# Kernel optimization log

Hardware: AMD Instinct MI355X
Metric: run time of the kernel (lower is better)

## Reference

```python
import jax, jax.numpy as jnp
import numpy as np

P, Q, R, H1, H2, PH, B = 32, 32, 8, 128, 64, 16, 8192
PAIRS = P * Q
OUT = PAIRS * R  # X_Z_layer output units


def _pairwise_mask(p, q, r):
    # rows i*q+k correspond to pair (x_i, z_k): connected to x_i and z_k only
    mx = np.zeros((p * q, p), np.float32)
    for i in range(p):
        mx[i * q:(i + 1) * q, i] = 1.0
    mz = np.tile(np.eye(q, dtype=np.float32), (p, 1))
    m = np.concatenate([mx, mz], axis=1)          # [p*q, p+q]
    return np.repeat(m, r, axis=0)                 # [p*q*r, p+q]


def setup_inputs() -> dict:
    key = jax.random.key(0)
    ks = jax.random.split(key, 24)
    rn = lambda k, s, sc=0.1: jax.random.normal(k, s, jnp.float32) * sc
    x = jax.random.normal(ks[0], (B, P), jnp.float32)
    z = jax.random.normal(ks[1], (B, Q), jnp.float32)
    # X_mlp: P -> H1 -> H2 -> 1
    xw1, xb1 = rn(ks[2], (P, H1)), rn(ks[3], (H1,))
    xw2, xb2 = rn(ks[4], (H1, H2)), rn(ks[5], (H2,))
    xw3, xb3 = rn(ks[6], (H2, 1)), rn(ks[7], (1,))
    # Z_mlp: Q -> H1 -> H2 -> 1
    zw1, zb1 = rn(ks[8], (Q, H1)), rn(ks[9], (H1,))
    zw2, zb2 = rn(ks[10], (Q if False else H1, H2)), rn(ks[11], (H2,))
    zw3, zb3 = rn(ks[12], (H2, 1)), rn(ks[13], (1,))
    # masked X_Z_layer: weight pre-multiplied by structured mask (as in __init__)
    mask = jnp.asarray(_pairwise_mask(P, Q, R))    # [OUT, P+Q]
    xzw = (rn(ks[14], (OUT, P + Q)) * mask).T      # [P+Q, OUT]
    xzb = rn(ks[15], (OUT,))
    # 1024 tiny per-pair MLPs: R -> PH (bias) -> 1 (no bias), stacked
    pw1 = rn(ks[16], (PAIRS, R, PH))
    pb1 = rn(ks[17], (PAIRS, PH))
    pw2 = rn(ks[18], (PAIRS, PH))
    return dict(x=x, z=z, xw1=xw1, xb1=xb1, xw2=xw2, xb2=xb2, xw3=xw3, xb3=xb3,
                zw1=zw1, zb1=zb1, zw2=zw2, zb2=zb2, zw3=zw3, zb3=zb3,
                xzw=xzw, xzb=xzb, pw1=pw1, pb1=pb1, pw2=pw2)


def reference(x, z, xw1, xb1, xw2, xb2, xw3, xb3,
              zw1, zb1, zw2, zb2, zw3, zb3, xzw, xzb, pw1, pb1, pw2):
    relu = jax.nn.relu
    # main-effect MLPs
    hx = relu(relu(x @ xw1 + xb1) @ xw2 + xb2)
    out_x = hx @ xw3 + xb3                         # [B,1]
    hz = relu(relu(z @ zw1 + zb1) @ zw2 + zb2)
    out_z = hz @ zw3 + zb3                         # [B,1]
    # masked interaction layer
    xz = jnp.concatenate([x, z], axis=1)           # [B, P+Q]
    h = relu(xz @ xzw + xzb)                       # [B, OUT]
    # all 1024 per-pair MLPs as one batched GEMM
    hp = h.reshape(h.shape[0], PAIRS, R)           # [B, pairs, R]
    t = relu(jnp.einsum('bpr,prh->bph', hp, pw1) + pb1)
    out_xz = jnp.einsum('bph,ph->b', t, pw2)[:, None]  # sum over pairs -> [B,1]
    return out_x + out_z + out_xz
```

## Files before the change

### kernel.cpp

```cpp
#include <hip/hip_runtime.h>

#define B_TOT 8192
#define PP 32
#define QQ 32
#define RR 8
#define H1 128
#define H2 64
#define PHH 16
#define PAIRS 1024
#define OUT_UNITS 8192

#define NBLK_MM 256
#define NBLK_IA 2048

typedef float f32x16 __attribute__((ext_vector_type(16)));
typedef short s16x8  __attribute__((ext_vector_type(8)));

union FragU { s16x8 v; unsigned int u[4]; };

__device__ inline unsigned int pack_bf16(float lo, float hi) {
    return __builtin_amdgcn_perm(__float_as_uint(hi), __float_as_uint(lo), 0x07060302u);
}

union SharedU {
    union {
        struct {
            float zT[16][256];
            float4 lwx[16][2];
            float4 lwz[16][2];
            float4 lhb[16][2];
            unsigned lpw1T[17][16][4];
            float lpb[16][16];
            float lpw2[16][16];
        } s;
        float red[256][33];
    } ia;
    struct {
        union {
            float xT[32][68];
            float h1T[128][68];
        };
    } mm;
};

__global__ __launch_bounds__(512, 4) void fused_k(
    const float* __restrict__ x, const float* __restrict__ z,
    const float* __restrict__ xw1, const float* __restrict__ xb1,
    const float* __restrict__ xw2, const float* __restrict__ xb2,
    const float* __restrict__ xw3, const float* __restrict__ xb3,
    const float* __restrict__ zw1, const float* __restrict__ zb1,
    const float* __restrict__ zw2, const float* __restrict__ zb2,
    const float* __restrict__ zw3, const float* __restrict__ zb3,
    const float* __restrict__ xzw, const float* __restrict__ xzb,
    const float* __restrict__ pw1, const float* __restrict__ pb1,
    const float* __restrict__ pw2, float* __restrict__ out)
{
    __shared__ SharedU sh;
    const int bid  = blockIdx.x;
    const int t    = threadIdx.x;
    const int w    = t >> 6;
    const int lane = t & 63;

    if (bid >= NBLK_MM) {
        const int ib    = bid - NBLK_MM;
        const int bx    = ib & 31;
        const int y     = ib >> 5;
        const int m     = lane & 31;
        const int kh    = lane >> 5;
        const int jj    = m & 15;
        const int cph   = m >> 4;
        const int b0    = bx * 256;
        const int i_x   = y >> 1;
        const int k0    = (y & 1) * 16;
        const int pair0 = y * 16;

        {
            int row = t >> 1;
            int c8  = (t & 1) * 8;
            const float* src = z + (size_t)(b0 + row) * 32 + k0 + c8;
            float4 a4 = *reinterpret_cast<const float4*>(src);
            float4 b4 = *reinterpret_cast<const float4*>(src + 4);
            sh.ia.s.zT[c8+0][row] = a4.x; sh.ia.s.zT[c8+1][row] = a4.y;
            sh.ia.s.zT[c8+2][row] = a4.z; sh.ia.s.zT[c8+3][row] = a4.w;
            sh.ia.s.zT[c8+4][row] = b4.x; sh.ia.s.zT[c8+5][row] = b4.y;
            sh.ia.s.zT[c8+6][row] = b4.z; sh.ia.s.zT[c8+7][row] = b4.w;
        }
        if (t < 128) {
            int p = t >> 3, c = t & 7;
            int gp = pair0 + p;
            reinterpret_cast<float*>(sh.ia.s.lwx)[t] = xzw[(size_t)i_x * OUT_UNITS + gp*8 + c];
            reinterpret_cast<float*>(sh.ia.s.lwz)[t] = xzw[(size_t)(32 + k0 + p) * OUT_UNITS + gp*8 + c];
            reinterpret_cast<float*>(sh.ia.s.lhb)[t] = xzb[gp*8 + c];
        }
        if (t < 256) {
            int p = t >> 4, j = t & 15;
            int gp = pair0 + p;
            sh.ia.s.lpb[p][j]  = pb1[gp*PHH + j];
            sh.ia.s.lpw2[p][j] = pw2[gp*PHH + j];
        }
        #pragma unroll
        for (int it = 0; it < 2; ++it) {
            int idx = t + it * 512;
            int p = idx >> 6, u = (idx >> 4) & 3, j = idx & 15;
            int gp = pair0 + p;
            float lo = pw1[(size_t)gp * 128 + (2*u)*16 + j];
            float hi = pw1[(size_t)gp * 128 + (2*u+1)*16 + j];
            sh.ia.s.lpw1T[p][j][u] = pack_bf16(lo, hi);
        }
        if (t < 64) reinterpret_cast<unsigned*>(sh.ia.s.lpw1T[16])[t] = 0u;

        const int g   = w >> 1;
        const int pph = w & 1;
        const int bl  = g * 64 + m;
        const float xv0 = x[(size_t)(b0 + bl)      * 32 + i_x];
        const float xv1 = x[(size_t)(b0 + bl + 32) * 32 + i_x];
        __syncthreads();

        f32x16 acc0, acc1;
        #pragma unroll
        for (int r = 0; r < 16; ++r) { acc0[r] = 0.f; acc1[r] = 0.f; }

        const bool realB = (kh == cph);

        #pragma unroll 2
        for (int kk = 0; kk < 4; ++kk) {
            const int ppl = pph * 4 + kk;
            const int pAl = 2*ppl + kh;
            const int pBl = 2*ppl + cph;

            const float zv0 = sh.ia.s.zT[pAl][bl];
            const float zv1 = sh.ia.s.zT[pAl][bl + 32];
            const float4 wxa = sh.ia.s.lwx[pAl][0], wxb = sh.ia.s.lwx[pAl][1];
            const float4 wza = sh.ia.s.lwz[pAl][0], wzb = sh.ia.s.lwz[pAl][1];
            const float4 hba = sh.ia.s.lhb[pAl][0], hbb = sh.ia.s.lhb[pAl][1];

            float h0[8], h1v[8];
            h0[0] = fmaxf(fmaf(xv0, wxa.x, fmaf(zv0, wza.x, hba.x)), 0.f);
            h0[1] = fmaxf(fmaf(xv0, wxa.y, fmaf(zv0, wza.y, hba.y)), 0.f);
            h0[2] = fmaxf(fmaf(xv0, wxa.z, fmaf(zv0, wza.z, hba.z)), 0.f);
            h0[3] = fmaxf(fmaf(xv0, wxa.w, fmaf(zv0, wza.w, hba.w)), 0.f);
            h0[4] = fmaxf(fmaf(xv0, wxb.x, fmaf(zv0, wzb.x, hbb.x)), 0.f);
            h0[5] = fmaxf(fmaf(xv0, wxb.y, fmaf(zv0, wzb.y, hbb.y)), 0.f);
            h0[6] = fmaxf(fmaf(xv0, wxb.z, fmaf(zv0, wzb.z, hbb.z)), 0.f);
            h0[7] = fmaxf(fmaf(xv0, wxb.w, fmaf(zv0, wzb.w, hbb.w)), 0.f);
            h1v[0] = fmaxf(fmaf(xv1, wxa.x, fmaf(zv1, wza.x, hba.x)), 0.f);
            h1v[1] = fmaxf(fmaf(xv1, wxa.y, fmaf(zv1, wza.y, hba.y)), 0.f);
            h1v[2] = fmaxf(fmaf(xv1, wxa.z, fmaf(zv1, wza.z, hba.z)), 0.f);
            h1v[3] = fmaxf(fmaf(xv1, wxa.w, fmaf(zv1, wza.w, hba.w)), 0.f);
            h1v[4] = fmaxf(fmaf(xv1, wxb.x, fmaf(zv1, wzb.x, hbb.x)), 0.f);
            h1v[5] = fmaxf(fmaf(xv1, wxb.y, fmaf(zv1, wzb.y, hbb.y)), 0.f);
            h1v[6] = fmaxf(fmaf(xv1, wxb.z, fmaf(zv1, wzb.z, hbb.z)), 0.f);
            h1v[7] = fmaxf(fmaf(xv1, wxb.w, fmaf(zv1, wzb.w, hbb.w)), 0.f);

            FragU a0, a1, bf;
            a0.u[0] = pack_bf16(h0[0], h0[1]);
            a0.u[1] = pack_bf16(h0[2], h0[3]);
            a0.u[2] = pack_bf16(h0[4], h0[5]);
            a0.u[3] = pack_bf16(h0[6], h0[7]);
            a1.u[0] = pack_bf16(h1v[0], h1v[1]);
            a1.u[1] = pack_bf16(h1v[2], h1v[3]);
            a1.u[2] = pack_bf16(h1v[4], h1v[5]);
            a1.u[3] = pack_bf16(h1v[6], h1v[7]);

            const unsigned* bq = sh.ia.s.lpw1T[realB ? pBl : 16][jj];
            bf.u[0] = bq[0]; bf.u[1] = bq[1]; bf.u[2] = bq[2]; bf.u[3] = bq[3];

            const float pbv = sh.ia.s.lpb[pBl][jj];
            const float w2v = sh.ia.s.lpw2[pBl][jj];

            f32x16 cpb;
            #pragma unroll
            for (int r = 0; r < 16; ++r) cpb[r] = pbv;

            f32x16 d0 = __builtin_amdgcn_mfma_f32_32x32x16_bf16(a0.v, bf.v, cpb, 0, 0, 0);
            f32x16 d1 = __builtin_amdgcn_mfma_f32_32x32x16_bf16(a1.v, bf.v, cpb, 0, 0, 0);

            #pragma unroll
            for (int r = 0; r < 16; ++r)
                acc0[r] = fmaf(fmaxf(d0[r], 0.f), w2v, acc0[r]);
            #pragma unroll
            for (int r = 0; r < 16; ++r)
                acc1[r] = fmaf(fmaxf(d1[r], 0.f), w2v, acc1[r]);
        }

        __syncthreads();
        const int rbase = g * 64;
        if (pph == 0) {
            #pragma unroll
            for (int r = 0; r < 16; ++r) {
                int rowf = (r & 3) + 8 * (r >> 2) + 4 * kh;
                sh.ia.red[rbase + rowf][m]      = acc0[r];
                sh.ia.red[rbase + 32 + rowf][m] = acc1[r];
            }
        }
        __syncthreads();
        if (pph == 1) {
            #pragma unroll
            for (int r = 0; r < 16; ++r) {
                int rowf = (r & 3) + 8 * (r >> 2) + 4 * kh;
                sh.ia.red[rbase + rowf][m]      += acc0[r];
                sh.ia.red[rbase + 32 + rowf][m] += acc1[r];
            }
        }
        __syncthreads();
        if (t < 256) {
            float s = 0.f;
            #pragma unroll
            for (int c = 0; c < 32; ++c) s += sh.ia.red[t][c];
            atomicAdd(out + b0 + t, s);
        }
    } else {
        const int btile = bid & 127;
        const int which = bid >> 7;
        const float* in = which ? z   : x;
        const float* w1 = which ? zw1 : xw1;
        const float* b1 = which ? zb1 : xb1;
        const float* w2 = which ? zw2 : xw2;
        const float* b2 = which ? zb2 : xb2;
        const float* w3 = which ? zw3 : xw3;
        const float* b3 = which ? zb3 : xb3;
        const int b0 = btile * 64;
        const int bw = w * 8;

        {
            int row = t >> 3;
            int c4  = (t & 7) * 4;
            float4 v = *reinterpret_cast<const float4*>(in + (size_t)(b0 + row) * 32 + c4);
            sh.mm.xT[c4+0][row] = v.x; sh.mm.xT[c4+1][row] = v.y;
            sh.mm.xT[c4+2][row] = v.z; sh.mm.xT[c4+3][row] = v.w;
        }
        __syncthreads();

        const int j1 = lane, j2 = lane + 64;
        float a1[8], a2[8];
        {
            float bb1 = b1[j1], bb2 = b1[j2];
            #pragma unroll
            for (int i = 0; i < 8; ++i) { a1[i] = bb1; a2[i] = bb2; }
        }
        #pragma unroll 4
        for (int m = 0; m < 32; ++m) {
            const float4* xr = reinterpret_cast<const float4*>(&sh.mm.xT[m][bw]);
            float4 xa = xr[0], xb = xr[1];
            float wv1 = w1[m*H1 + j1];
            float wv2 = w1[m*H1 + j2];
            a1[0] = fmaf(xa.x, wv1, a1[0]); a2[0] = fmaf(xa.x, wv2, a2[0]);
            a1[1] = fmaf(xa.y, wv1, a1[1]); a2[1] = fmaf(xa.y, wv2, a2[1]);
            a1[2] = fmaf(xa.z, wv1, a1[2]); a2[2] = fmaf(xa.z, wv2, a2[2]);
            a1[3] = fmaf(xa.w, wv1, a1[3]); a2[3] = fmaf(xa.w, wv2, a2[3]);
            a1[4] = fmaf(xb.x, wv1, a1[4]); a2[4] = fmaf(xb.x, wv2, a2[4]);
            a1[5] = fmaf(xb.y, wv1, a1[5]); a2[5] = fmaf(xb.y, wv2, a2[5]);
            a1[6] = fmaf(xb.z, wv1, a1[6]); a2[6] = fmaf(xb.z, wv2, a2[6]);
            a1[7] = fmaf(xb.w, wv1, a1[7]); a2[7] = fmaf(xb.w, wv2, a2[7]);
        }
        __syncthreads();
        #pragma unroll
        for (int i = 0; i < 8; ++i) {
            sh.mm.h1T[j1][bw + i] = fmaxf(a1[i], 0.f);
            sh.mm.h1T[j2][bw + i] = fmaxf(a2[i], 0.f);
        }
        __syncthreads();

        float hacc[8];
        {
            float b2v = b2[lane];
            #pragma unroll
            for (int i = 0; i < 8; ++i) hacc[i] = b2v;
        }
        #pragma unroll 4
        for (int m = 0; m < 128; ++m) {
            float w2v = w2[m*H2 + lane];
            const float4* hr = reinterpret_cast<const float4*>(&sh.mm.h1T[m][bw]);
            float4 ha = hr[0], hb = hr[1];
            hacc[0] = fmaf(ha.x, w2v, hacc[0]);
            hacc[1] = fmaf(ha.y, w2v, hacc[1]);
            hacc[2] = fmaf(ha.z, w2v, hacc[2]);
            hacc[3] = fmaf(ha.w, w2v, hacc[3]);
            hacc[4] = fmaf(hb.x, w2v, hacc[4]);
            hacc[5] = fmaf(hb.y, w2v, hacc[5]);
            hacc[6] = fmaf(hb.z, w2v, hacc[6]);
            hacc[7] = fmaf(hb.w, w2v, hacc[7]);
        }
        {
            float w3v = w3[lane];
            #pragma unroll
            for (int i = 0; i < 8; ++i) hacc[i] = fmaxf(hacc[i], 0.f) * w3v;
        }
        __syncthreads();
        #pragma unroll
        for (int i = 0; i < 8; ++i)
            sh.mm.h1T[bw + i][lane] = hacc[i];
        __syncthreads();
        if (t < 64) {
            float s = b3[0];
            const float4* rr = reinterpret_cast<const float4*>(&sh.mm.h1T[t][0]);
            #pragma unroll
            for (int c = 0; c < 16; ++c) {
                float4 v = rr[c];
                s += (v.x + v.y) + (v.z + v.w);
            }
            atomicAdd(out + b0 + t, s);
        }
    }
}

extern "C" void kernel_launch(void* const* d_in, const int* in_sizes, int n_in,
                              void* d_out, int out_size, void* d_ws, size_t ws_size,
                              hipStream_t stream) {
    const float* x   = (const float*)d_in[0];
    const float* z   = (const float*)d_in[1];
    const float* xw1 = (const float*)d_in[2];
    const float* xb1 = (const float*)d_in[3];
    const float* xw2 = (const float*)d_in[4];
    const float* xb2 = (const float*)d_in[5];
    const float* xw3 = (const float*)d_in[6];
    const float* xb3 = (const float*)d_in[7];
    const float* zw1 = (const float*)d_in[8];
    const float* zb1 = (const float*)d_in[9];
    const float* zw2 = (const float*)d_in[10];
    const float* zb2 = (const float*)d_in[11];
    const float* zw3 = (const float*)d_in[12];
    const float* zb3 = (const float*)d_in[13];
    const float* xzw = (const float*)d_in[14];
    const float* xzb = (const float*)d_in[15];
    const float* pw1 = (const float*)d_in[16];
    const float* pb1 = (const float*)d_in[17];
    const float* pw2 = (const float*)d_in[18];
    float* out = (float*)d_out;

    hipMemsetAsync(out, 0, (size_t)out_size * sizeof(float), stream);

    fused_k<<<dim3(NBLK_MM + NBLK_IA), 512, 0, stream>>>(
        x, z, xw1, xb1, xw2, xb2, xw3, xb3,
        zw1, zb1, zw2, zb2, zw3, zb3,
        xzw, xzb, pw1, pb1, pw2, out);
}
```

Baseline: 124.8 us.

## Give each wave its own batch rows, use hardware bf16 pack, raise occupancy

The interaction path is remapped so each of the eight waves handles 32 batch rows over all 8 pair-groups, instead of two waves splitting the pair range over 64 rows. This removes the two-phase shared-memory accumulate of partial sums between wave pairs, and halves the per-thread accumulator registers. The bf16 packing switches from a truncating byte permute to the v_cvt_pk_bf16_f32 instruction, which rounds instead of truncating and may cost slightly differently. The launch bound asks for 6 blocks per CU instead of 4, which caps registers per thread and risks spills.

```diff
diff --git a/kernel.cpp b/kernel.cpp
--- a/kernel.cpp
+++ b/kernel.cpp
@@ -19,7 +19,9 @@
 union FragU { s16x8 v; unsigned int u[4]; };
 
 __device__ inline unsigned int pack_bf16(float lo, float hi) {
-    return __builtin_amdgcn_perm(__float_as_uint(hi), __float_as_uint(lo), 0x07060302u);
+    unsigned int r;
+    asm("v_cvt_pk_bf16_f32 %0, %1, %2" : "=v"(r) : "v"(lo), "v"(hi));
+    return r;
 }
 
 union SharedU {
@@ -43,7 +45,7 @@
     } mm;
 };
 
-__global__ __launch_bounds__(512, 4) void fused_k(
+__global__ __launch_bounds__(512, 6) void fused_k(
     const float* __restrict__ x, const float* __restrict__ z,
     const float* __restrict__ xw1, const float* __restrict__ xb1,
     const float* __restrict__ xw2, const float* __restrict__ xb2,
@@ -109,58 +111,41 @@
         }
         if (t < 64) reinterpret_cast<unsigned*>(sh.ia.s.lpw1T[16])[t] = 0u;
 
-        const int g   = w >> 1;
-        const int pph = w & 1;
-        const int bl  = g * 64 + m;
-        const float xv0 = x[(size_t)(b0 + bl)      * 32 + i_x];
-        const float xv1 = x[(size_t)(b0 + bl + 32) * 32 + i_x];
-        __syncthreads();
-
-        f32x16 acc0, acc1;
-        #pragma unroll
-        for (int r = 0; r < 16; ++r) { acc0[r] = 0.f; acc1[r] = 0.f; }
+        const int bl = w * 32 + m;
+        const float xv = x[(size_t)(b0 + bl) * 32 + i_x];
+        __syncthreads();
+
+        f32x16 acc;
+        #pragma unroll
+        for (int r = 0; r < 16; ++r) acc[r] = 0.f;
 
         const bool realB = (kh == cph);
 
         #pragma unroll 2
-        for (int kk = 0; kk < 4; ++kk) {
-            const int ppl = pph * 4 + kk;
+        for (int ppl = 0; ppl < 8; ++ppl) {
             const int pAl = 2*ppl + kh;
             const int pBl = 2*ppl + cph;
 
-            const float zv0 = sh.ia.s.zT[pAl][bl];
-            const float zv1 = sh.ia.s.zT[pAl][bl + 32];
+            const float zv = sh.ia.s.zT[pAl][bl];
             const float4 wxa = sh.ia.s.lwx[pAl][0], wxb = sh.ia.s.lwx[pAl][1];
             const float4 wza = sh.ia.s.lwz[pAl][0], wzb = sh.ia.s.lwz[pAl][1];
             const float4 hba = sh.ia.s.lhb[pAl][0], hbb = sh.ia.s.lhb[pAl][1];
 
-            float h0[8], h1v[8];
-            h0[0] = fmaxf(fmaf(xv0, wxa.x, fmaf(zv0, wza.x, hba.x)), 0.f);
-            h0[1] = fmaxf(fmaf(xv0, wxa.y, fmaf(zv0, wza.y, hba.y)), 0.f);
-            h0[2] = fmaxf(fmaf(xv0, wxa.z, fmaf(zv0, wza.z, hba.z)), 0.f);
-            h0[3] = fmaxf(fmaf(xv0, wxa.w, fmaf(zv0, wza.w, hba.w)), 0.f);
-            h0[4] = fmaxf(fmaf(xv0, wxb.x, fmaf(zv0, wzb.x, hbb.x)), 0.f);
-            h0[5] = fmaxf(fmaf(xv0, wxb.y, fmaf(zv0, wzb.y, hbb.y)), 0.f);
-            h0[6] = fmaxf(fmaf(xv0, wxb.z, fmaf(zv0, wzb.z, hbb.z)), 0.f);
-            h0[7] = fmaxf(fmaf(xv0, wxb.w, fmaf(zv0, wzb.w, hbb.w)), 0.f);
-            h1v[0] = fmaxf(fmaf(xv1, wxa.x, fmaf(zv1, wza.x, hba.x)), 0.f);
-            h1v[1] = fmaxf(fmaf(xv1, wxa.y, fmaf(zv1, wza.y, hba.y)), 0.f);
-            h1v[2] = fmaxf(fmaf(xv1, wxa.z, fmaf(zv1, wza.z, hba.z)), 0.f);
-            h1v[3] = fmaxf(fmaf(xv1, wxa.w, fmaf(zv1, wza.w, hba.w)), 0.f);
-            h1v[4] = fmaxf(fmaf(xv1, wxb.x, fmaf(zv1, wzb.x, hbb.x)), 0.f);
-            h1v[5] = fmaxf(fmaf(xv1, wxb.y, fmaf(zv1, wzb.y, hbb.y)), 0.f);
-            h1v[6] = fmaxf(fmaf(xv1, wxb.z, fmaf(zv1, wzb.z, hbb.z)), 0.f);
-            h1v[7] = fmaxf(fmaf(xv1, wxb.w, fmaf(zv1, wzb.w, hbb.w)), 0.f);
-
-            FragU a0, a1, bf;
+            float h0[8];
+            h0[0] = fmaxf(fmaf(xv, wxa.x, fmaf(zv, wza.x, hba.x)), 0.f);
+            h0[1] = fmaxf(fmaf(xv, wxa.y, fmaf(zv, wza.y, hba.y)), 0.f);
+            h0[2] = fmaxf(fmaf(xv, wxa.z, fmaf(zv, wza.z, hba.z)), 0.f);
+            h0[3] = fmaxf(fmaf(xv, wxa.w, fmaf(zv, wza.w, hba.w)), 0.f);
+            h0[4] = fmaxf(fmaf(xv, wxb.x, fmaf(zv, wzb.x, hbb.x)), 0.f);
+            h0[5] = fmaxf(fmaf(xv, wxb.y, fmaf(zv, wzb.y, hbb.y)), 0.f);
+            h0[6] = fmaxf(fmaf(xv, wxb.z, fmaf(zv, wzb.z, hbb.z)), 0.f);
+            h0[7] = fmaxf(fmaf(xv, wxb.w, fmaf(zv, wzb.w, hbb.w)), 0.f);
+
+            FragU a0, bf;
             a0.u[0] = pack_bf16(h0[0], h0[1]);
             a0.u[1] = pack_bf16(h0[2], h0[3]);
             a0.u[2] = pack_bf16(h0[4], h0[5]);
             a0.u[3] = pack_bf16(h0[6], h0[7]);
-            a1.u[0] = pack_bf16(h1v[0], h1v[1]);
-            a1.u[1] = pack_bf16(h1v[2], h1v[3]);
-            a1.u[2] = pack_bf16(h1v[4], h1v[5]);
-            a1.u[3] = pack_bf16(h1v[6], h1v[7]);
 
             const unsigned* bq = sh.ia.s.lpw1T[realB ? pBl : 16][jj];
             bf.u[0] = bq[0]; bf.u[1] = bq[1]; bf.u[2] = bq[2]; bf.u[3] = bq[3];
@@ -172,35 +157,18 @@
             #pragma unroll
             for (int r = 0; r < 16; ++r) cpb[r] = pbv;
 
-            f32x16 d0 = __builtin_amdgcn_mfma_f32_32x32x16_bf16(a0.v, bf.v, cpb, 0, 0, 0);
-            f32x16 d1 = __builtin_amdgcn_mfma_f32_32x32x16_bf16(a1.v, bf.v, cpb, 0, 0, 0);
+            f32x16 d = __builtin_amdgcn_mfma_f32_32x32x16_bf16(a0.v, bf.v, cpb, 0, 0, 0);
 
             #pragma unroll
             for (int r = 0; r < 16; ++r)
-                acc0[r] = fmaf(fmaxf(d0[r], 0.f), w2v, acc0[r]);
-            #pragma unroll
-            for (int r = 0; r < 16; ++r)
-                acc1[r] = fmaf(fmaxf(d1[r], 0.f), w2v, acc1[r]);
-        }
-
-        __syncthreads();
-        const int rbase = g * 64;
-        if (pph == 0) {
-            #pragma unroll
-            for (int r = 0; r < 16; ++r) {
-                int rowf = (r & 3) + 8 * (r >> 2) + 4 * kh;
-                sh.ia.red[rbase + rowf][m]      = acc0[r];
-                sh.ia.red[rbase + 32 + rowf][m] = acc1[r];
-            }
-        }
-        __syncthreads();
-        if (pph == 1) {
-            #pragma unroll
-            for (int r = 0; r < 16; ++r) {
-                int rowf = (r & 3) + 8 * (r >> 2) + 4 * kh;
-                sh.ia.red[rbase + rowf][m]      += acc0[r];
-                sh.ia.red[rbase + 32 + rowf][m] += acc1[r];
-            }
+                acc[r] = fmaf(fmaxf(d[r], 0.f), w2v, acc[r]);
+        }
+
+        __syncthreads();
+        #pragma unroll
+        for (int r = 0; r < 16; ++r) {
+            int rowf = (r & 3) + 8 * (r >> 2) + 4 * kh;
+            sh.ia.red[w * 32 + rowf][m] = acc[r];
         }
         __syncthreads();
         if (t < 256) {
```

Measured after the change: 118.7 us. 4.9% less time.
